# Optimization experiments

Hardware: AMD Instinct MI355X
Metric: run time of the kernel (lower is better)

## Reference

```python
import jax, jax.numpy as jnp
import numpy as np

B, NS, H = 131072, 64, 32
# e3nn path normalization (irrep_normalization='component', path_normalization='element')
PW1_0 = float((NS * NS + 25.0) ** -0.5)            # paths into hidden 0e: sqrt(1/(NS^2 + 5*5))
PW1_2 = float((5.0 / (10.0 * NS + 25.0)) ** 0.5)   # paths into hidden 2e: sqrt(5/(NS*5 + 5*NS + 25))
PW2_2 = float((5.0 / (3.0 * H * H)) ** 0.5)        # paths into output 2e: sqrt(5/(3*H^2))
INV_S5 = float(5.0 ** -0.5)                        # w3j(0,2,2) = delta/sqrt(5); w3j(2,2,0) = delta/sqrt(5)

def _wigner3j_222():
    # Real l=2 basis as orthonormal symmetric traceless 3x3 matrices (tr(Ma Mb)=delta).
    # C_abc = tr(sym(Ma Mb) Mc), fully symmetric invariant 3-tensor, Frobenius-normalized to 1
    # (the real Wigner 3j for (2,2,2), up to basis orientation convention).
    s2, s6 = np.sqrt(2.0), np.sqrt(6.0)
    M = np.zeros((5, 3, 3))
    M[0] = np.array([[0., 1, 0], [1, 0, 0], [0, 0, 0]]) / s2   # xy
    M[1] = np.array([[0., 0, 0], [0, 0, 1], [0, 1, 0]]) / s2   # yz
    M[2] = np.diag([-1., -1, 2]) / s6                           # 2z^2-x^2-y^2
    M[3] = np.array([[0., 0, 1], [0, 0, 0], [1, 0, 0]]) / s2   # xz
    M[4] = np.diag([1., -1, 0]) / s2                            # x^2-y^2
    C = np.einsum('aij,bjk,cki->abc', M, M, M)
    C = 0.5 * (C + C.transpose(1, 0, 2))
    return C / np.linalg.norm(C)

C222 = jnp.asarray(_wigner3j_222(), dtype=jnp.float32)

def setup_inputs() -> dict:
    key = jax.random.key(0)
    ks = jax.random.split(key, 14)
    f = jnp.float32
    return {
        'scalars': jax.random.normal(ks[0], (B, NS), f),
        'kernel_t2_sum': jax.random.normal(ks[1], (B, 5), f),
        'mc_t2': jax.random.normal(ks[2], (B, 5), f),
        'coulomb_t2': jax.random.normal(ks[3], (B, 5), f),
        'bs_t2': jax.random.normal(ks[4], (B, 5), f),
        'mopac_coulomb_t2': jax.random.normal(ks[5], (B, 5), f),
        # tp1 weights (e3nn internal weights ~ N(0,1)), one (mul1,mul2,mul_out) block per path
        'w1_sss': jax.random.normal(ks[6], (NS, NS, H), f),   # 0e x 0e -> 0e
        'w1_stt': jax.random.normal(ks[7], (NS, 5, H), f),    # 0e x 2e -> 2e
        'w1_tst': jax.random.normal(ks[8], (5, NS, H), f),    # 2e x 0e -> 2e
        'w1_tts': jax.random.normal(ks[9], (5, 5, H), f),     # 2e x 2e -> 0e
        'w1_ttt': jax.random.normal(ks[10], (5, 5, H), f),    # 2e x 2e -> 2e
        # tp2 weights
        'w2_stt': jax.random.normal(ks[11], (H, H, 1), f),
        'w2_tst': jax.random.normal(ks[12], (H, H, 1), f),
        'w2_ttt': jax.random.normal(ks[13], (H, H, 1), f),
    }

def _forward(scalars, kernel_t2_sum, mc_t2, coulomb_t2, bs_t2, mopac_coulomb_t2,
             w1_sss, w1_stt, w1_tst, w1_tts, w1_ttt, w2_stt, w2_tst, w2_ttt):
    s = scalars                                                        # (B, NS) : NS x 0e
    t = jnp.stack([kernel_t2_sum, mc_t2, coulomb_t2, bs_t2,
                   mopac_coulomb_t2], axis=1)
    # tp1: x (x) x -> hidden (H x 0e + H x 2e)
    h_s = PW1_0 * (jnp.einsum('uvw,bu,bv->bw', w1_sss, s, s)
                   + INV_S5 * jnp.einsum('uvw,bui,bvi->bw', w1_tts, t, t))          # (B, H)
    h_t = PW1_2 * (INV_S5 * jnp.einsum('uvw,bu,bvk->bwk', w1_stt, s, t)
                   + INV_S5 * jnp.einsum('uvw,buk,bv->bwk', w1_tst, t, s)
                   + jnp.einsum('uvw,ijk,bui,bvj->bwk', w1_ttt, C222, t, t))        # (B, H, 5)
    out = PW2_2 * (INV_S5 * jnp.einsum('uvw,bu,bvk->bwk', w2_stt, h_s, h_t)
                   + INV_S5 * jnp.einsum('uvw,buk,bv->bwk', w2_tst, h_t, h_s)
                   + jnp.einsum('uvw,ijk,bui,bvj->bwk', w2_ttt, C222, h_t, h_t))    # (B, 1, 5)
    return out[:, 0, :]                                                             # (B, 5)

def reference(scalars, kernel_t2_sum, mc_t2, coulomb_t2, bs_t2, mopac_coulomb_t2,
              w1_sss, w1_stt, w1_tst, w1_tts, w1_ttt, w2_stt, w2_tst, w2_ttt):
    return _forward(scalars, kernel_t2_sum, mc_t2, coulomb_t2, bs_t2, mopac_coulomb_t2,
                    w1_sss, w1_stt, w1_tst, w1_tts, w1_ttt, w2_stt, w2_tst, w2_ttt)
```

## Files before the change

### kernel.cpp

```cpp
#include <hip/hip_runtime.h>
#include <math.h>
#include <stdint.h>


#define CW1 0.23904572186687872f
#define CW2 0.20701966780270626f
#define CW3 0.11952286093343936f

typedef float f32x4 __attribute__((ext_vector_type(4)));
typedef short bf16x8 __attribute__((ext_vector_type(8)));
typedef uint32_t u32x4 __attribute__((ext_vector_type(4)));

__device__ __forceinline__ uint32_t f2bf(float f) {
  uint32_t x = __float_as_uint(f);
  return (x + 0x7fffu + ((x >> 16) & 1u)) >> 16;
}
__device__ __forceinline__ uint32_t packbf(float lo, float hi) {
  return f2bf(lo) | (f2bf(hi) << 16);
}
__device__ __forceinline__ float bflo(uint32_t d) { return __uint_as_float(d << 16); }
__device__ __forceinline__ float bfhi(uint32_t d) { return __uint_as_float(d & 0xffff0000u); }
__device__ __forceinline__ float bfval(uint32_t h) { return __uint_as_float(h << 16); }

#define MF16(a, b, c) __builtin_amdgcn_mfma_f32_16x16x32_bf16((a), (b), (c), 0, 0, 0)

__device__ __align__(16) uint32_t g_bsss16[64 * 2 * 2 * 64 * 4];
__device__ __align__(16) uint32_t g_bst16[5 * 2 * 2 * 64 * 4];
__device__ __align__(16) uint32_t g_btts16[2 * 64 * 4];
__device__ __align__(16) uint32_t g_bttt16[2 * 64 * 4];
__device__ __align__(16) uint32_t g_bg2_16[2 * 64 * 4];
__device__ __align__(16) uint32_t g_bgt16[2 * 64 * 4];

__device__ const int c_pu[16] = {0,0,0,0,0,1,1,1,1,2,2,2,3,3,4,0};
__device__ const int c_pv[16] = {0,1,2,3,4,1,2,3,4,2,3,4,3,4,4,0};

__global__ void ech_prep(const float* __restrict__ w1_sss, const float* __restrict__ w1_stt,
                         const float* __restrict__ w1_tst, const float* __restrict__ w1_tts,
                         const float* __restrict__ w1_ttt, const float* __restrict__ w2_stt,
                         const float* __restrict__ w2_tst, const float* __restrict__ w2_ttt) {
  const float PW1_0 = (float)(1.0 / sqrt(4121.0));
  const float PW1_2 = (float)sqrt(5.0 / 665.0);
  const float PW2_2 = (float)sqrt(5.0 / 3072.0);
  const float IS5   = (float)sqrt(0.2);

  int idx = blockIdx.x * 256 + threadIdx.x;

  if (idx < 65536) {
    int d = idx & 3, l = (idx >> 2) & 63, c = (idx >> 8) & 1, n = (idx >> 9) & 1, v = idx >> 10;
    int gg = l >> 4, w = n * 16 + (l & 15);
    int u0 = 32 * c + 8 * gg + 2 * d, u1 = u0 + 1;
    float lo = 0.f, hi = 0.f;
    if (u0 < v)       lo = w1_sss[(u0 * 64 + v) * 32 + w] + w1_sss[(v * 64 + u0) * 32 + w];
    else if (u0 == v) lo = w1_sss[(u0 * 64 + v) * 32 + w];
    if (u1 < v)       hi = w1_sss[(u1 * 64 + v) * 32 + w] + w1_sss[(v * 64 + u1) * 32 + w];
    else if (u1 == v) hi = w1_sss[(u1 * 64 + v) * 32 + w];
    g_bsss16[idx] = packbf(PW1_0 * lo, PW1_0 * hi);
    return;
  }
  idx -= 65536;
  if (idx < 5120) {
    int d = idx & 3, l = (idx >> 2) & 63, c = (idx >> 8) & 1, n = (idx >> 9) & 1, ct = idx >> 10;
    int gg = l >> 4, w = n * 16 + (l & 15);
    float sc = PW1_2 * IS5;
    int u0 = 32 * c + 8 * gg + 2 * d, u1 = u0 + 1;
    g_bst16[idx] = packbf(sc * (w1_stt[(u0 * 5 + ct) * 32 + w] + w1_tst[(ct * 64 + u0) * 32 + w]),
                          sc * (w1_stt[(u1 * 5 + ct) * 32 + w] + w1_tst[(ct * 64 + u1) * 32 + w]));
    return;
  }
  idx -= 5120;
  if (idx < 512) {
    int d = idx & 3, l = (idx >> 2) & 63, n = idx >> 8;
    int gg = l >> 4, w = n * 16 + (l & 15);
    float sc = PW1_0 * IS5;
    float val[2];
#pragma unroll
    for (int q = 0; q < 2; ++q) {
      int p = 8 * gg + 2 * d + q;
      float x = 0.f;
      if (p < 15) {
        int u = c_pu[p], v = c_pv[p];
        x = w1_tts[(u * 5 + v) * 32 + w];
        if (u < v) x += w1_tts[(v * 5 + u) * 32 + w];
        x *= sc;
      }
      val[q] = x;
    }
    g_btts16[idx] = packbf(val[0], val[1]);
    return;
  }
  idx -= 512;
  if (idx < 512) {
    int d = idx & 3, l = (idx >> 2) & 63, n = idx >> 8;
    int gg = l >> 4, w = n * 16 + (l & 15);
    float val[2];
#pragma unroll
    for (int q = 0; q < 2; ++q) {
      int p = 8 * gg + 2 * d + q;
      float x = 0.f;
      if (p < 15) {
        int u = c_pu[p], v = c_pv[p];
        x = w1_ttt[(u * 5 + v) * 32 + w];
        if (u < v) x += w1_ttt[(v * 5 + u) * 32 + w];
        x *= PW1_2;
      }
      val[q] = x;
    }
    g_bttt16[idx] = packbf(val[0], val[1]);
    return;
  }
  idx -= 512;
  if (idx < 512) {
    int d = idx & 3, l = (idx >> 2) & 63, n = idx >> 8;
    int gg = l >> 4, v = n * 16 + (l & 15);
    float sc = PW2_2 * IS5;
    int u0 = 8 * gg + 2 * d, u1 = u0 + 1;
    g_bg2_16[idx] = packbf(sc * (w2_stt[u0 * 32 + v] + w2_tst[v * 32 + u0]),
                           sc * (w2_stt[u1 * 32 + v] + w2_tst[v * 32 + u1]));
    return;
  }
  idx -= 512;
  if (idx < 512) {
    int d = idx & 3, l = (idx >> 2) & 63, n = idx >> 8;
    int gg = l >> 4, v = n * 16 + (l & 15);
    int u0 = 8 * gg + 2 * d, u1 = u0 + 1;
    g_bgt16[idx] = packbf(PW2_2 * w2_ttt[u0 * 32 + v], PW2_2 * w2_ttt[u1 * 32 + v]);
    return;
  }
}

#define S_STRIDE 67
#define OFF_T 4288
#define ED_STRIDE 49
#define PLANE(i) ((i) * 1088)
#define LDS_DW 6592

__global__ __launch_bounds__(256, 2)
void ech_fused(const float* __restrict__ scalars,
               const float* __restrict__ tk, const float* __restrict__ tm,
               const float* __restrict__ tc, const float* __restrict__ tb,
               const float* __restrict__ tmc,
               float* __restrict__ out) {
  __shared__ uint32_t lds[LDS_DW];

  const int tid = threadIdx.x;
  const int rows64 = blockIdx.x * 64;
  const int wave = tid >> 6, lane = tid & 63;
  const int g = lane >> 4, col16 = lane & 15;
  const int wrow = wave * 16;
  const f32x4 zero4 = {0.f, 0.f, 0.f, 0.f};

#pragma unroll
  for (int it = 0; it < 8; ++it) {
    int di = it * 256 + tid;
    int row = di >> 5, j = di & 31;
    float f0 = scalars[(rows64 + row) * 64 + 2 * j];
    float f1 = scalars[(rows64 + row) * 64 + 2 * j + 1];
    uint32_t h0 = f2bf(f0), h1 = f2bf(f1);
    float r0 = f0 - bfval(h0), r1 = f1 - bfval(h1);
    lds[row * S_STRIDE + 2 * j]     = h0 | (h1 << 16);
    lds[row * S_STRIDE + 2 * j + 1] = f2bf(r0) | (f2bf(r1) << 16);
  }
#pragma unroll
  for (int v = 0; v < 5; ++v) {
    const float* p = (v == 0 ? tk : v == 1 ? tm : v == 2 ? tc : v == 3 ? tb : tmc);
#pragma unroll
    for (int it = 0; it < 2; ++it) {
      int i = it * 256 + tid;
      if (i < 320)
        lds[OFF_T + (i / 5) * 25 + v * 5 + (i % 5)] = __float_as_uint(p[rows64 * 5 + i]);
    }
  }
  __syncthreads();

  bf16x8 afr_hi[2], afr_lo[2];
#pragma unroll
  for (int c = 0; c < 2; ++c) {
    int base = (wrow + col16) * S_STRIDE + 32 * c + 8 * g;
    u32x4 th, tl;
    th.x = lds[base + 0]; tl.x = lds[base + 1];
    th.y = lds[base + 2]; tl.y = lds[base + 3];
    th.z = lds[base + 4]; tl.z = lds[base + 5];
    th.w = lds[base + 6]; tl.w = lds[base + 7];
    afr_hi[c] = __builtin_bit_cast(bf16x8, th);
    afr_lo[c] = __builtin_bit_cast(bf16x8, tl);
  }

  f32x4 hsA = zero4, hsB = zero4;
  const bf16x8* gb = (const bf16x8*)g_bsss16;
#pragma unroll 2
  for (int vd = 0; vd < 16; ++vd) {
    int v0 = 2 * vd, v1 = v0 + 1;
    bf16x8 b00 = gb[(v0 * 4 + 0) * 64 + lane];
    bf16x8 b01 = gb[(v0 * 4 + 2) * 64 + lane];
    bf16x8 b10 = gb[(v1 * 4 + 0) * 64 + lane];
    bf16x8 b11 = gb[(v1 * 4 + 2) * 64 + lane];
    f32x4 Z00 = zero4, Z01 = zero4, Z10 = zero4, Z11 = zero4;
    Z00 = MF16(afr_hi[0], b00, Z00); Z00 = MF16(afr_lo[0], b00, Z00);
    Z01 = MF16(afr_hi[0], b01, Z01); Z01 = MF16(afr_lo[0], b01, Z01);
    Z10 = MF16(afr_hi[0], b10, Z10); Z10 = MF16(afr_lo[0], b10, Z10);
    Z11 = MF16(afr_hi[0], b11, Z11); Z11 = MF16(afr_lo[0], b11, Z11);
#pragma unroll
    for (int r = 0; r < 4; ++r) {
      int row = wrow + 4 * g + r;
      uint32_t dh = lds[row * S_STRIDE + 2 * vd];
      uint32_t dl = lds[row * S_STRIDE + 2 * vd + 1];
      float s0 = bflo(dh) + bflo(dl);
      float s1 = bfhi(dh) + bfhi(dl);
      hsA[r] = fmaf(s0, Z00[r], hsA[r]); hsA[r] = fmaf(s1, Z10[r], hsA[r]);
      hsB[r] = fmaf(s0, Z01[r], hsB[r]); hsB[r] = fmaf(s1, Z11[r], hsB[r]);
    }
  }
#pragma unroll 2
  for (int vd = 16; vd < 32; ++vd) {
    int v0 = 2 * vd, v1 = v0 + 1;
    f32x4 Z00 = zero4, Z01 = zero4, Z10 = zero4, Z11 = zero4;
#pragma unroll
    for (int c = 0; c < 2; ++c) {
      bf16x8 b00 = gb[(v0 * 4 + 0 + c) * 64 + lane];
      bf16x8 b01 = gb[(v0 * 4 + 2 + c) * 64 + lane];
      bf16x8 b10 = gb[(v1 * 4 + 0 + c) * 64 + lane];
      bf16x8 b11 = gb[(v1 * 4 + 3 - 1 + c - c) * 64 + lane];
      b11 = gb[(v1 * 4 + 2 + c) * 64 + lane];
      Z00 = MF16(afr_hi[c], b00, Z00); Z00 = MF16(afr_lo[c], b00, Z00);
      Z01 = MF16(afr_hi[c], b01, Z01); Z01 = MF16(afr_lo[c], b01, Z01);
      Z10 = MF16(afr_hi[c], b10, Z10); Z10 = MF16(afr_lo[c], b10, Z10);
      Z11 = MF16(afr_hi[c], b11, Z11); Z11 = MF16(afr_lo[c], b11, Z11);
    }
#pragma unroll
    for (int r = 0; r < 4; ++r) {
      int row = wrow + 4 * g + r;
      uint32_t dh = lds[row * S_STRIDE + 2 * vd];
      uint32_t dl = lds[row * S_STRIDE + 2 * vd + 1];
      float s0 = bflo(dh) + bflo(dl);
      float s1 = bfhi(dh) + bfhi(dl);
      hsA[r] = fmaf(s0, Z00[r], hsA[r]); hsA[r] = fmaf(s1, Z10[r], hsA[r]);
      hsB[r] = fmaf(s0, Z01[r], hsB[r]); hsB[r] = fmaf(s1, Z11[r], hsB[r]);
    }
  }

  f32x4 ht[5][2];
#pragma unroll
  for (int k = 0; k < 5; ++k) { ht[k][0] = zero4; ht[k][1] = zero4; }
  {
    const bf16x8* gs = (const bf16x8*)g_bst16;
#pragma unroll
    for (int ct = 0; ct < 5; ++ct) {
      f32x4 a0 = zero4, a1 = zero4;
#pragma unroll
      for (int c = 0; c < 2; ++c) {
        bf16x8 b0 = gs[(ct * 4 + 0 + c) * 64 + lane];
        bf16x8 b1 = gs[(ct * 4 + 2 + c) * 64 + lane];
        a0 = MF16(afr_hi[c], b0, a0); a0 = MF16(afr_lo[c], b0, a0);
        a1 = MF16(afr_hi[c], b1, a1); a1 = MF16(afr_lo[c], b1, a1);
      }
#pragma unroll
      for (int r = 0; r < 4; ++r) {
        int row = wrow + 4 * g + r;
        int tbi = OFF_T + row * 25 + ct * 5;
        float t0 = __uint_as_float(lds[tbi + 0]);
        float t1 = __uint_as_float(lds[tbi + 1]);
        float t2 = __uint_as_float(lds[tbi + 2]);
        float t3 = __uint_as_float(lds[tbi + 3]);
        float t4 = __uint_as_float(lds[tbi + 4]);
        ht[0][0][r] = fmaf(a0[r], t0, ht[0][0][r]); ht[0][1][r] = fmaf(a1[r], t0, ht[0][1][r]);
        ht[1][0][r] = fmaf(a0[r], t1, ht[1][0][r]); ht[1][1][r] = fmaf(a1[r], t1, ht[1][1][r]);
        ht[2][0][r] = fmaf(a0[r], t2, ht[2][0][r]); ht[2][1][r] = fmaf(a1[r], t2, ht[2][1][r]);
        ht[3][0][r] = fmaf(a0[r], t3, ht[3][0][r]); ht[3][1][r] = fmaf(a1[r], t3, ht[3][1][r]);
        ht[4][0][r] = fmaf(a0[r], t4, ht[4][0][r]); ht[4][1][r] = fmaf(a1[r], t4, ht[4][1][r]);
      }
    }
  }
  __syncthreads();

  {
    int row = tid >> 2, part = tid & 3;
    int tbase = OFF_T + row * 25;
    float P[4][6];
#pragma unroll
    for (int q = 0; q < 4; ++q) {
      int p = part * 4 + q;
      int U = c_pu[p], V = c_pv[p];
      float a0 = __uint_as_float(lds[tbase + U * 5 + 0]);
      float a1 = __uint_as_float(lds[tbase + U * 5 + 1]);
      float a2 = __uint_as_float(lds[tbase + U * 5 + 2]);
      float a3 = __uint_as_float(lds[tbase + U * 5 + 3]);
      float a4 = __uint_as_float(lds[tbase + U * 5 + 4]);
      float b0 = __uint_as_float(lds[tbase + V * 5 + 0]);
      float b1 = __uint_as_float(lds[tbase + V * 5 + 1]);
      float b2 = __uint_as_float(lds[tbase + V * 5 + 2]);
      float b3 = __uint_as_float(lds[tbase + V * 5 + 3]);
      float b4 = __uint_as_float(lds[tbase + V * 5 + 4]);
      float d0 = a0 * b0, d1 = a1 * b1, d2 = a2 * b2, d3 = a3 * b3, d4 = a4 * b4;
      float s01 = a0 * b1 + a1 * b0;
      float s02 = a0 * b2 + a2 * b0;
      float s03 = a0 * b3 + a3 * b0;
      float s12 = a1 * b2 + a2 * b1;
      float s13 = a1 * b3 + a3 * b1;
      float s14 = a1 * b4 + a4 * b1;
      float s23 = a2 * b3 + a3 * b2;
      float s24 = a2 * b4 + a4 * b2;
      float s34 = a3 * b4 + a4 * b3;
      P[q][0] = -CW1 * s02 + CW2 * s13;
      P[q][1] = CW2 * s03 + CW3 * s12 - CW2 * s14;
      P[q][2] = -CW1 * d0 + CW3 * d1 + CW1 * d2 + CW3 * d3 - CW1 * d4;
      P[q][3] = CW2 * s01 + CW3 * s23 + CW2 * s34;
      P[q][4] = -CW2 * d1 - CW1 * s24 + CW2 * d3;
      P[q][5] = d0 + d1 + d2 + d3 + d4;
      if (p == 15) {
#pragma unroll
        for (int c6 = 0; c6 < 6; ++c6) P[q][c6] = 0.f;
      }
    }
    int rb = row * ED_STRIDE + part * 2;
#pragma unroll
    for (int comp = 0; comp < 6; ++comp) {
      lds[rb + comp * 8 + 0] = packbf(P[0][comp], P[1][comp]);
      lds[rb + comp * 8 + 1] = packbf(P[2][comp], P[3][comp]);
    }
  }
  __syncthreads();

  {
    int arow = wrow + col16;
    int gl = g & 1;
    bool gok = (g < 2);
    {
      int b5 = arow * ED_STRIDE + 40 + 4 * gl;
      u32x4 tmp;
      tmp.x = gok ? lds[b5 + 0] : 0u;
      tmp.y = gok ? lds[b5 + 1] : 0u;
      tmp.z = gok ? lds[b5 + 2] : 0u;
      tmp.w = gok ? lds[b5 + 3] : 0u;
      bf16x8 dfr = __builtin_bit_cast(bf16x8, tmp);
      hsA = MF16(dfr, ((const bf16x8*)g_btts16)[lane], hsA);
      hsB = MF16(dfr, ((const bf16x8*)g_btts16)[64 + lane], hsB);
    }
    bf16x8 btt0 = ((const bf16x8*)g_bttt16)[lane];
    bf16x8 btt1 = ((const bf16x8*)g_bttt16)[64 + lane];
#pragma unroll
    for (int k = 0; k < 5; ++k) {
      int bk = arow * ED_STRIDE + k * 8 + 4 * gl;
      u32x4 tmp;
      tmp.x = gok ? lds[bk + 0] : 0u;
      tmp.y = gok ? lds[bk + 1] : 0u;
      tmp.z = gok ? lds[bk + 2] : 0u;
      tmp.w = gok ? lds[bk + 3] : 0u;
      bf16x8 efr = __builtin_bit_cast(bf16x8, tmp);
      ht[k][0] = MF16(efr, btt0, ht[k][0]);
      ht[k][1] = MF16(efr, btt1, ht[k][1]);
    }
  }
  __syncthreads();

#pragma unroll
  for (int r = 0; r < 4; ++r) {
    int row = wrow + 4 * g + r;
    int dwb = row * 17 + (col16 >> 1);
    float pA = __shfl_xor(hsA[r], 1, 64);
    float pB = __shfl_xor(hsB[r], 1, 64);
    if (!(col16 & 1)) {
      lds[PLANE(0) + dwb]     = packbf(hsA[r], pA);
      lds[PLANE(0) + dwb + 8] = packbf(hsB[r], pB);
    }
#pragma unroll
    for (int k = 0; k < 5; ++k) {
      float qA = __shfl_xor(ht[k][0][r], 1, 64);
      float qB = __shfl_xor(ht[k][1][r], 1, 64);
      if (!(col16 & 1)) {
        lds[PLANE(1 + k) + dwb]     = packbf(ht[k][0][r], qA);
        lds[PLANE(1 + k) + dwb + 8] = packbf(ht[k][1][r], qB);
      }
    }
  }

  f32x4 g2n[2];
  {
    int prow = wrow + col16;
    int b = PLANE(0) + prow * 17 + 4 * g;
    u32x4 tmp;
    tmp.x = lds[b]; tmp.y = lds[b + 1]; tmp.z = lds[b + 2]; tmp.w = lds[b + 3];
    bf16x8 af = __builtin_bit_cast(bf16x8, tmp);
    g2n[0] = MF16(af, ((const bf16x8*)g_bg2_16)[lane], zero4);
    g2n[1] = MF16(af, ((const bf16x8*)g_bg2_16)[64 + lane], zero4);
  }
  f32x4 gt[5][2];
#pragma unroll
  for (int i = 0; i < 5; ++i) {
    int prow = wrow + col16;
    int b = PLANE(1 + i) + prow * 17 + 4 * g;
    u32x4 tmp;
    tmp.x = lds[b]; tmp.y = lds[b + 1]; tmp.z = lds[b + 2]; tmp.w = lds[b + 3];
    bf16x8 af = __builtin_bit_cast(bf16x8, tmp);
    gt[i][0] = MF16(af, ((const bf16x8*)g_bgt16)[lane], zero4);
    gt[i][1] = MF16(af, ((const bf16x8*)g_bgt16)[64 + lane], zero4);
  }

#define REDSTORE(K)                                                        \
  {                                                                        \
    _Pragma("unroll") for (int m = 1; m <= 8; m <<= 1)                     \
        _Pragma("unroll") for (int r = 0; r < 4; ++r)                      \
            tot[r] += __shfl_xor(tot[r], m, 64);                           \
    if (col16 == (K)) {                                                    \
      _Pragma("unroll") for (int r = 0; r < 4; ++r)                        \
          out[(size_t)(rows64 + wrow + 4 * g + r) * 5 + (K)] = tot[r];     \
    }                                                                      \
  }

  {
    float tot[4];
#pragma unroll
    for (int r = 0; r < 4; ++r) {
      float s = 0.f;
#pragma unroll
      for (int n = 0; n < 2; ++n) {
        float ok = g2n[n][r] * ht[0][n][r];
        ok = fmaf(-CW1, gt[0][n][r] * ht[2][n][r] + gt[2][n][r] * ht[0][n][r], ok);
        ok = fmaf( CW2, gt[1][n][r] * ht[3][n][r] + gt[3][n][r] * ht[1][n][r], ok);
        s += ok;
      }
      tot[r] = s;
    }
    REDSTORE(0)
  }
  {
    float tot[4];
#pragma unroll
    for (int r = 0; r < 4; ++r) {
      float s = 0.f;
#pragma unroll
      for (int n = 0; n < 2; ++n) {
        float ok = g2n[n][r] * ht[1][n][r];
        ok = fmaf( CW2, gt[0][n][r] * ht[3][n][r] + gt[3][n][r] * ht[0][n][r], ok);
        ok = fmaf( CW3, gt[1][n][r] * ht[2][n][r] + gt[2][n][r] * ht[1][n][r], ok);
        ok = fmaf(-CW2, gt[1][n][r] * ht[4][n][r] + gt[4][n][r] * ht[1][n][r], ok);
        s += ok;
      }
      tot[r] = s;
    }
    REDSTORE(1)
  }
  {
    float tot[4];
#pragma unroll
    for (int r = 0; r < 4; ++r) {
      float s = 0.f;
#pragma unroll
      for (int n = 0; n < 2; ++n) {
        float ok = g2n[n][r] * ht[2][n][r];
        ok = fmaf(-CW1, gt[0][n][r] * ht[0][n][r], ok);
        ok = fmaf( CW3, gt[1][n][r] * ht[1][n][r], ok);
        ok = fmaf( CW1, gt[2][n][r] * ht[2][n][r], ok);
        ok = fmaf( CW3, gt[3][n][r] * ht[3][n][r], ok);
        ok = fmaf(-CW1, gt[4][n][r] * ht[4][n][r], ok);
        s += ok;
      }
      tot[r] = s;
    }
    REDSTORE(2)
  }
  {
    float tot[4];
#pragma unroll
    for (int r = 0; r < 4; ++r) {
      float s = 0.f;
#pragma unroll
      for (int n = 0; n < 2; ++n) {
        float ok = g2n[n][r] * ht[3][n][r];
        ok = fmaf( CW2, gt[0][n][r] * ht[1][n][r] + gt[1][n][r] * ht[0][n][r], ok);
        ok = fmaf( CW3, gt[2][n][r] * ht[3][n][r] + gt[3][n][r] * ht[2][n][r], ok);
        ok = fmaf( CW2, gt[3][n][r] * ht[4][n][r] + gt[4][n][r] * ht[3][n][r], ok);
        s += ok;
      }
      tot[r] = s;
    }
    REDSTORE(3)
  }
  {
    float tot[4];
#pragma unroll
    for (int r = 0; r < 4; ++r) {
      float s = 0.f;
#pragma unroll
      for (int n = 0; n < 2; ++n) {
        float ok = g2n[n][r] * ht[4][n][r];
        ok = fmaf(-CW2, gt[1][n][r] * ht[1][n][r], ok);
        ok = fmaf(-CW1, gt[2][n][r] * ht[4][n][r] + gt[4][n][r] * ht[2][n][r], ok);
        ok = fmaf( CW2, gt[3][n][r] * ht[3][n][r], ok);
        s += ok;
      }
      tot[r] = s;
    }
    REDSTORE(4)
  }
}

extern "C" void kernel_launch(void* const* d_in, const int* in_sizes, int n_in,
                              void* d_out, int out_size, void* d_ws, size_t ws_size,
                              hipStream_t stream) {
  (void)n_in; (void)out_size; (void)d_ws; (void)ws_size;
  const float* scalars = (const float*)d_in[0];
  const float* tk  = (const float*)d_in[1];
  const float* tm  = (const float*)d_in[2];
  const float* tc  = (const float*)d_in[3];
  const float* tb  = (const float*)d_in[4];
  const float* tmc = (const float*)d_in[5];

  ech_prep<<<284, 256, 0, stream>>>((const float*)d_in[6], (const float*)d_in[7],
                                    (const float*)d_in[8], (const float*)d_in[9],
                                    (const float*)d_in[10], (const float*)d_in[11],
                                    (const float*)d_in[12], (const float*)d_in[13]);

  const int B = in_sizes[0] / 64;
  ech_fused<<<B / 64, 256, 0, stream>>>(scalars, tk, tm, tc, tb, tmc, (float*)d_out);
}
```

Measured before the change: 107.2 us.

## Stage w1_sss B-fragments into LDS via async global_load_lds double buffering

The hs contraction loop used to load its B fragments directly from global memory into registers in every iteration. It now streams the g_bsss16 weight blocks into a double-buffered LDS staging area with async global_load_lds, prefetching the next chunk while MFMAs run on the current one. A block barrier is added per chunk. LDS use grows from about 26KB to about 56KB per block, which may limit occupancy with launch_bounds(256,2).

```diff
diff --git a/kernel.cpp b/kernel.cpp
--- a/kernel.cpp
+++ b/kernel.cpp
@@ -10,6 +10,9 @@
 typedef float f32x4 __attribute__((ext_vector_type(4)));
 typedef short bf16x8 __attribute__((ext_vector_type(8)));
 typedef uint32_t u32x4 __attribute__((ext_vector_type(4)));
+
+typedef const __attribute__((address_space(1))) uint32_t* gas1p;
+typedef __attribute__((address_space(3))) uint32_t* las3p;
 
 __device__ __forceinline__ uint32_t f2bf(float f) {
   uint32_t x = __float_as_uint(f);
@@ -130,9 +133,14 @@
 
 #define S_STRIDE 67
 #define OFF_T 4288
+#define OFF_STG 5888
 #define ED_STRIDE 49
 #define PLANE(i) ((i) * 1088)
-#define LDS_DW 6592
+#define LDS_DW 14080
+
+__device__ __forceinline__ void gld16(const uint32_t* gsrc, uint32_t* ldst) {
+  __builtin_amdgcn_global_load_lds((gas1p)gsrc, (las3p)ldst, 16, 0, 0);
+}
 
 __global__ __launch_bounds__(256, 2)
 void ech_fused(const float* __restrict__ scalars,
@@ -170,6 +178,11 @@
         lds[OFF_T + (i / 5) * 25 + v * 5 + (i % 5)] = __float_as_uint(p[rows64 * 5 + i]);
     }
   }
+#pragma unroll
+  for (int ro = 0; ro < 2; ++ro) {
+    int slot = ro * 4 + wave;
+    gld16(g_bsss16 + slot * 512 + lane * 4, lds + OFF_STG + slot * 256 + lane * 4);
+  }
   __syncthreads();
 
   bf16x8 afr_hi[2], afr_lo[2];
@@ -186,56 +199,84 @@
   }
 
   f32x4 hsA = zero4, hsB = zero4;
-  const bf16x8* gb = (const bf16x8*)g_bsss16;
-#pragma unroll 2
-  for (int vd = 0; vd < 16; ++vd) {
-    int v0 = 2 * vd, v1 = v0 + 1;
-    bf16x8 b00 = gb[(v0 * 4 + 0) * 64 + lane];
-    bf16x8 b01 = gb[(v0 * 4 + 2) * 64 + lane];
-    bf16x8 b10 = gb[(v1 * 4 + 0) * 64 + lane];
-    bf16x8 b11 = gb[(v1 * 4 + 2) * 64 + lane];
-    f32x4 Z00 = zero4, Z01 = zero4, Z10 = zero4, Z11 = zero4;
-    Z00 = MF16(afr_hi[0], b00, Z00); Z00 = MF16(afr_lo[0], b00, Z00);
-    Z01 = MF16(afr_hi[0], b01, Z01); Z01 = MF16(afr_lo[0], b01, Z01);
-    Z10 = MF16(afr_hi[0], b10, Z10); Z10 = MF16(afr_lo[0], b10, Z10);
-    Z11 = MF16(afr_hi[0], b11, Z11); Z11 = MF16(afr_lo[0], b11, Z11);
-#pragma unroll
-    for (int r = 0; r < 4; ++r) {
-      int row = wrow + 4 * g + r;
-      uint32_t dh = lds[row * S_STRIDE + 2 * vd];
-      uint32_t dl = lds[row * S_STRIDE + 2 * vd + 1];
-      float s0 = bflo(dh) + bflo(dl);
-      float s1 = bfhi(dh) + bfhi(dl);
-      hsA[r] = fmaf(s0, Z00[r], hsA[r]); hsA[r] = fmaf(s1, Z10[r], hsA[r]);
-      hsB[r] = fmaf(s0, Z01[r], hsB[r]); hsB[r] = fmaf(s1, Z11[r], hsB[r]);
-    }
-  }
-#pragma unroll 2
-  for (int vd = 16; vd < 32; ++vd) {
-    int v0 = 2 * vd, v1 = v0 + 1;
-    f32x4 Z00 = zero4, Z01 = zero4, Z10 = zero4, Z11 = zero4;
-#pragma unroll
-    for (int c = 0; c < 2; ++c) {
-      bf16x8 b00 = gb[(v0 * 4 + 0 + c) * 64 + lane];
-      bf16x8 b01 = gb[(v0 * 4 + 2 + c) * 64 + lane];
-      bf16x8 b10 = gb[(v1 * 4 + 0 + c) * 64 + lane];
-      bf16x8 b11 = gb[(v1 * 4 + 3 - 1 + c - c) * 64 + lane];
-      b11 = gb[(v1 * 4 + 2 + c) * 64 + lane];
-      Z00 = MF16(afr_hi[c], b00, Z00); Z00 = MF16(afr_lo[c], b00, Z00);
-      Z01 = MF16(afr_hi[c], b01, Z01); Z01 = MF16(afr_lo[c], b01, Z01);
-      Z10 = MF16(afr_hi[c], b10, Z10); Z10 = MF16(afr_lo[c], b10, Z10);
-      Z11 = MF16(afr_hi[c], b11, Z11); Z11 = MF16(afr_lo[c], b11, Z11);
-    }
-#pragma unroll
-    for (int r = 0; r < 4; ++r) {
-      int row = wrow + 4 * g + r;
-      uint32_t dh = lds[row * S_STRIDE + 2 * vd];
-      uint32_t dl = lds[row * S_STRIDE + 2 * vd + 1];
-      float s0 = bflo(dh) + bflo(dl);
-      float s1 = bfhi(dh) + bfhi(dl);
-      hsA[r] = fmaf(s0, Z00[r], hsA[r]); hsA[r] = fmaf(s1, Z10[r], hsA[r]);
-      hsB[r] = fmaf(s0, Z01[r], hsB[r]); hsB[r] = fmaf(s1, Z11[r], hsB[r]);
-    }
+#pragma unroll 1
+  for (int ch = 0; ch < 16; ++ch) {
+    uint32_t* bufc = lds + OFF_STG + (ch & 1) * 4096;
+    if (ch < 15) {
+      int cn = ch + 1;
+      uint32_t* bufn = lds + OFF_STG + (cn & 1) * 4096;
+      if (cn < 8) {
+#pragma unroll
+        for (int ro = 0; ro < 2; ++ro) {
+          int slot = ro * 4 + wave;
+          gld16(g_bsss16 + cn * 4096 + slot * 512 + lane * 4,
+                bufn + slot * 256 + lane * 4);
+        }
+      } else {
+#pragma unroll
+        for (int ro = 0; ro < 4; ++ro) {
+          int slot = ro * 4 + wave;
+          gld16(g_bsss16 + cn * 4096 + slot * 256 + lane * 4,
+                bufn + slot * 256 + lane * 4);
+        }
+      }
+    }
+    if (ch < 8) {
+#pragma unroll
+      for (int vin = 0; vin < 4; ++vin) {
+        int v = ch * 4 + vin;
+        const uint32_t* p0 = bufc + (vin * 2 + 0) * 256 + lane * 4;
+        const uint32_t* p1 = bufc + (vin * 2 + 1) * 256 + lane * 4;
+        u32x4 t0, t1;
+        t0.x = p0[0]; t0.y = p0[1]; t0.z = p0[2]; t0.w = p0[3];
+        t1.x = p1[0]; t1.y = p1[1]; t1.z = p1[2]; t1.w = p1[3];
+        bf16x8 b0 = __builtin_bit_cast(bf16x8, t0);
+        bf16x8 b1 = __builtin_bit_cast(bf16x8, t1);
+        f32x4 Z0 = MF16(afr_hi[0], b0, zero4); Z0 = MF16(afr_lo[0], b0, Z0);
+        f32x4 Z1 = MF16(afr_hi[0], b1, zero4); Z1 = MF16(afr_lo[0], b1, Z1);
+#pragma unroll
+        for (int r = 0; r < 4; ++r) {
+          int row = wrow + 4 * g + r;
+          uint32_t dh = lds[row * S_STRIDE + (v & ~1)];
+          uint32_t dl = lds[row * S_STRIDE + (v & ~1) + 1];
+          float sv = ((vin & 1) ? bfhi(dh) : bflo(dh)) + ((vin & 1) ? bfhi(dl) : bflo(dl));
+          hsA[r] = fmaf(sv, Z0[r], hsA[r]);
+          hsB[r] = fmaf(sv, Z1[r], hsB[r]);
+        }
+      }
+    } else {
+#pragma unroll
+      for (int vin = 0; vin < 4; ++vin) {
+        int v = ch * 4 + vin;
+        const uint32_t* p0 = bufc + (vin * 4 + 0) * 256 + lane * 4;
+        const uint32_t* pc = bufc + (vin * 4 + 1) * 256 + lane * 4;
+        const uint32_t* p1 = bufc + (vin * 4 + 2) * 256 + lane * 4;
+        const uint32_t* pd = bufc + (vin * 4 + 3) * 256 + lane * 4;
+        u32x4 t0, tc_, t1, td;
+        t0.x = p0[0]; t0.y = p0[1]; t0.z = p0[2]; t0.w = p0[3];
+        tc_.x = pc[0]; tc_.y = pc[1]; tc_.z = pc[2]; tc_.w = pc[3];
+        t1.x = p1[0]; t1.y = p1[1]; t1.z = p1[2]; t1.w = p1[3];
+        td.x = pd[0]; td.y = pd[1]; td.z = pd[2]; td.w = pd[3];
+        bf16x8 b0 = __builtin_bit_cast(bf16x8, t0);
+        bf16x8 bc = __builtin_bit_cast(bf16x8, tc_);
+        bf16x8 b1 = __builtin_bit_cast(bf16x8, t1);
+        bf16x8 bd = __builtin_bit_cast(bf16x8, td);
+        f32x4 Z0 = MF16(afr_hi[0], b0, zero4); Z0 = MF16(afr_lo[0], b0, Z0);
+        Z0 = MF16(afr_hi[1], bc, Z0);          Z0 = MF16(afr_lo[1], bc, Z0);
+        f32x4 Z1 = MF16(afr_hi[0], b1, zero4); Z1 = MF16(afr_lo[0], b1, Z1);
+        Z1 = MF16(afr_hi[1], bd, Z1);          Z1 = MF16(afr_lo[1], bd, Z1);
+#pragma unroll
+        for (int r = 0; r < 4; ++r) {
+          int row = wrow + 4 * g + r;
+          uint32_t dh = lds[row * S_STRIDE + (v & ~1)];
+          uint32_t dl = lds[row * S_STRIDE + (v & ~1) + 1];
+          float sv = ((vin & 1) ? bfhi(dh) : bflo(dh)) + ((vin & 1) ? bfhi(dl) : bflo(dl));
+          hsA[r] = fmaf(sv, Z0[r], hsA[r]);
+          hsB[r] = fmaf(sv, Z1[r], hsB[r]);
+        }
+      }
+    }
+    __syncthreads();
   }
 
   f32x4 ht[5][2];
```

Result: slower. 112.1 us (+4.6%).
